# Kernel tuning notes

Hardware: AMD Instinct MI355X
Metric: run time of the kernel (lower is better)

## Reference

```python
import jax, jax.numpy as jnp
import numpy as np
import itertools

N_LEVELS = 16
F = 2
OFFSETS = [0, 4096, 12096, 27721, 60489, 124489, 249489, 511633, 1023633,
           1547921, 2072209, 2596497, 3120785, 3645073, 4169361, 4693649, 5217937]
RESOLUTIONS = [16, 20, 25, 32, 40, 50, 64, 80, 101, 128, 161, 203, 256, 322, 406, 512]
# Instant-NGP spatial hash primes (first prime = 1)
PRIMES = np.array([1, 2654435761, 805459861], dtype=np.uint32)
CORNERS = np.array(list(itertools.product([0, 1], repeat=3)), dtype=np.int32)  # (8,3)
B = 1 << 20


def setup_inputs() -> dict:
    key = jax.random.key(0)
    k1, k2 = jax.random.split(key)
    xyz = jax.random.uniform(k1, (B, 3), dtype=jnp.float32)  # points in [0,1)
    embeddings = jax.random.normal(k2, (OFFSETS[-1], F), dtype=jnp.float32) * 0.01
    return {
        'xyz': xyz,
        'embeddings': embeddings,
        'min_xyz': jnp.zeros((3,), jnp.float32),
        'max_xyz': jnp.ones((3,), jnp.float32),
    }


def _hashgrid_encode(xyz, embeddings, min_xyz, max_xyz):
    # normalize to [0,1] inside the grid bbox
    xyz_n = (xyz - min_xyz) / (max_xyz - min_xyz)  # (B,3)
    corners_u = jnp.asarray(CORNERS).astype(jnp.uint32)          # (8,3)
    corners_f = jnp.asarray(CORNERS).astype(jnp.float32)         # (8,3)
    primes = jnp.asarray(PRIMES)                                  # (3,) uint32
    outs = []
    for l in range(N_LEVELS):
        res = RESOLUTIONS[l]
        size = OFFSETS[l + 1] - OFFSETS[l]
        pos = xyz_n * (res - 1)                                   # (B,3) in [0,res-1]
        pos0 = jnp.clip(jnp.floor(pos), 0.0, res - 2)             # lower corner
        w = pos - pos0                                            # (B,3) trilinear frac
        p0 = pos0.astype(jnp.uint32)
        idx3 = p0[:, None, :] + corners_u[None]                   # (B,8,3)
        if res ** 3 <= size:
            # dense level: linear index
            idx = idx3[..., 0] * jnp.uint32(res * res) + idx3[..., 1] * jnp.uint32(res) + idx3[..., 2]
        else:
            # hashed level: xor of prime-multiplied coords (uint32 wraparound)
            idx = (idx3[..., 0] * primes[0]) ^ (idx3[..., 1] * primes[1]) ^ (idx3[..., 2] * primes[2])
            idx = idx % jnp.uint32(size)
        idx = idx.astype(jnp.int32) + OFFSETS[l]                  # (B,8) global entry id
        # trilinear weights: prod_d [ c_d ? w_d : 1-w_d ]
        wc = jnp.prod(corners_f[None] * w[:, None, :] + (1.0 - corners_f[None]) * (1.0 - w[:, None, :]), axis=-1)  # (B,8)
        feats = embeddings[idx]                                   # (B,8,F) gather
        outs.append(jnp.einsum('bc,bcf->bf', wc, feats))          # (B,F)
    return jnp.concatenate(outs, axis=-1)                         # (B, L*F)


def reference(xyz, embeddings, min_xyz, max_xyz):
    return _hashgrid_encode(xyz, embeddings, min_xyz, max_xyz)
```

## Files before the change

kernel.cpp:

```cpp
#include <hip/hip_runtime.h>
#include <stdint.h>


__device__ __constant__ int kRES[16] = {16,20,25,32,40,50,64,80,101,128,161,203,256,322,406,512};

__global__ __launch_bounds__(256, 8) void hashgrid_phased(
    const float* __restrict__ xyz,
    const float2* __restrict__ emb,
    const float* __restrict__ mn,
    const float* __restrict__ mx,
    float* __restrict__ out,
    int npts)
{
    constexpr uint32_t P1 = 2654435761u, P2 = 805459861u;
    constexpr uint32_t HASH_MASK = 0x7FFFFu;
    constexpr uint32_t HASH_BASE = 1023633u;

    const int b = blockIdx.x * blockDim.x + threadIdx.x;
    if (b >= npts) return;

    const float mn0 = mn[0], mn1 = mn[1], mn2 = mn[2];
    const float inv0 = 1.0f / (mx[0] - mn0);
    const float inv1 = 1.0f / (mx[1] - mn1);
    const float inv2 = 1.0f / (mx[2] - mn2);

    const float xn = (xyz[3*b+0] - mn0) * inv0;
    const float yn = (xyz[3*b+1] - mn1) * inv1;
    const float zn = (xyz[3*b+2] - mn2) * inv2;

    const int y = blockIdx.y;

    if (y == 0) {
        constexpr int RES[8] = {16,20,25,32,40,50,64,80};
        constexpr uint32_t OFFS[8] = {0u,4096u,12096u,27721u,60489u,124489u,249489u,511633u};
        float o[16];
#pragma unroll
        for (int l = 0; l < 8; ++l) {
            const int res = RES[l];
            const uint32_t off = OFFS[l];
            const float scale = (float)(res - 1);
            const float hi = (float)(res - 2);

            const float px = xn * scale, py = yn * scale, pz = zn * scale;
            const float fx = fminf(fmaxf(floorf(px), 0.0f), hi);
            const float fy = fminf(fmaxf(floorf(py), 0.0f), hi);
            const float fz = fminf(fmaxf(floorf(pz), 0.0f), hi);
            const float wx1 = px - fx, wy1 = py - fy, wz1 = pz - fz;
            const float wx0 = 1.0f - wx1, wy0 = 1.0f - wy1, wz0 = 1.0f - wz1;
            const uint32_t ix = (uint32_t)fx, iy = (uint32_t)fy, iz = (uint32_t)fz;

            const uint32_t dx = (uint32_t)(res * res);
            const uint32_t dy = (uint32_t)res;
            const uint32_t base = off + ix * dx + iy * dy + iz;

            float ax = 0.0f, ay = 0.0f;
            {
                float2 e0 = emb[base];           float2 e1 = emb[base + 1];
                float wxy = wx0 * wy0;
                ax += wxy * (wz0 * e0.x + wz1 * e1.x);
                ay += wxy * (wz0 * e0.y + wz1 * e1.y);
            }
            {
                float2 e0 = emb[base + dy];      float2 e1 = emb[base + dy + 1];
                float wxy = wx0 * wy1;
                ax += wxy * (wz0 * e0.x + wz1 * e1.x);
                ay += wxy * (wz0 * e0.y + wz1 * e1.y);
            }
            {
                float2 e0 = emb[base + dx];      float2 e1 = emb[base + dx + 1];
                float wxy = wx1 * wy0;
                ax += wxy * (wz0 * e0.x + wz1 * e1.x);
                ay += wxy * (wz0 * e0.y + wz1 * e1.y);
            }
            {
                float2 e0 = emb[base + dx + dy]; float2 e1 = emb[base + dx + dy + 1];
                float wxy = wx1 * wy1;
                ax += wxy * (wz0 * e0.x + wz1 * e1.x);
                ay += wxy * (wz0 * e0.y + wz1 * e1.y);
            }
            o[2*l]   = ax;
            o[2*l+1] = ay;
        }
        float4* ov = (float4*)(out + (size_t)b * 32);
#pragma unroll
        for (int i = 0; i < 4; ++i)
            ov[i] = make_float4(o[4*i+0], o[4*i+1], o[4*i+2], o[4*i+3]);
    } else {
        const int l = y + 7;
        const int res = kRES[l];
        const uint32_t off = HASH_BASE + (uint32_t)(l - 8) * 524288u;

        const float scale = (float)(res - 1);
        const float hi = (float)(res - 2);

        const float px = xn * scale, py = yn * scale, pz = zn * scale;
        const float fx = fminf(fmaxf(floorf(px), 0.0f), hi);
        const float fy = fminf(fmaxf(floorf(py), 0.0f), hi);
        const float fz = fminf(fmaxf(floorf(pz), 0.0f), hi);
        const float wx1 = px - fx, wy1 = py - fy, wz1 = pz - fz;
        const float wx0 = 1.0f - wx1, wy0 = 1.0f - wy1, wz0 = 1.0f - wz1;
        const uint32_t ix = (uint32_t)fx, iy = (uint32_t)fy, iz = (uint32_t)fz;

        const uint32_t hx0 = ix,      hx1 = ix + 1u;
        const uint32_t hy0 = iy * P1, hy1 = hy0 + P1;
        const uint32_t hz0 = iz * P2, hz1 = hz0 + P2;

        const uint32_t i000 = ((hx0 ^ hy0 ^ hz0) & HASH_MASK) + off;
        const uint32_t i001 = ((hx0 ^ hy0 ^ hz1) & HASH_MASK) + off;
        const uint32_t i010 = ((hx0 ^ hy1 ^ hz0) & HASH_MASK) + off;
        const uint32_t i011 = ((hx0 ^ hy1 ^ hz1) & HASH_MASK) + off;
        const uint32_t i100 = ((hx1 ^ hy0 ^ hz0) & HASH_MASK) + off;
        const uint32_t i101 = ((hx1 ^ hy0 ^ hz1) & HASH_MASK) + off;
        const uint32_t i110 = ((hx1 ^ hy1 ^ hz0) & HASH_MASK) + off;
        const uint32_t i111 = ((hx1 ^ hy1 ^ hz1) & HASH_MASK) + off;

        float2 e000 = emb[i000], e001 = emb[i001], e010 = emb[i010], e011 = emb[i011];
        float2 e100 = emb[i100], e101 = emb[i101], e110 = emb[i110], e111 = emb[i111];

        float ax, ay, w;
        w = wx0*wy0*wz0; ax  = w*e000.x; ay  = w*e000.y;
        w = wx0*wy0*wz1; ax += w*e001.x; ay += w*e001.y;
        w = wx0*wy1*wz0; ax += w*e010.x; ay += w*e010.y;
        w = wx0*wy1*wz1; ax += w*e011.x; ay += w*e011.y;
        w = wx1*wy0*wz0; ax += w*e100.x; ay += w*e100.y;
        w = wx1*wy0*wz1; ax += w*e101.x; ay += w*e101.y;
        w = wx1*wy1*wz0; ax += w*e110.x; ay += w*e110.y;
        w = wx1*wy1*wz1; ax += w*e111.x; ay += w*e111.y;

        float2* op = (float2*)(out + (size_t)b * 32 + 2 * l);
        *op = make_float2(ax, ay);
    }
}

extern "C" void kernel_launch(void* const* d_in, const int* in_sizes, int n_in,
                              void* d_out, int out_size, void* d_ws, size_t ws_size,
                              hipStream_t stream) {
    const float*  xyz = (const float*)d_in[0];
    const float2* emb = (const float2*)d_in[1];
    const float*  mn  = (const float*)d_in[2];
    const float*  mx  = (const float*)d_in[3];
    float* out = (float*)d_out;

    const int npts = in_sizes[0] / 3;
    const int block = 256;
    const int grid_x = (npts + block - 1) / block;

    hipLaunchKernelGGL(hashgrid_phased, dim3(grid_x, 9), dim3(block), 0, stream,
                       xyz, emb, mn, mx, out, npts);
}
```

Measured before the change: 776.9 us.

## Repack dense-level embeddings into per-cell contiguous blocks before gathering

```diff
diff --git a/kernel.cpp b/kernel.cpp
--- a/kernel.cpp
+++ b/kernel.cpp
@@ -2,9 +2,166 @@
 #include <stdint.h>
 
 
+typedef float vf4 __attribute__((ext_vector_type(4)));
+typedef float vf2 __attribute__((ext_vector_type(2)));
+
 __device__ __constant__ int kRES[16] = {16,20,25,32,40,50,64,80,101,128,161,203,256,322,406,512};
 
-__global__ __launch_bounds__(256, 8) void hashgrid_phased(
+#define D_RES   {16,20,25,32,40,50,64,80}
+#define D_OFF   {0u,4096u,12096u,27721u,60489u,124489u,249489u,511633u}
+#define D_CBASE {0u,3375u,10234u,24058u,53849u,113168u,230817u,480864u}
+#define D_CTOT  973903u
+#define D_QTOT  3895612u
+
+__device__ __constant__ uint32_t kCB[9] = {0u,3375u,10234u,24058u,53849u,113168u,230817u,480864u,973903u};
+__device__ __constant__ int      kDR[8] = D_RES;
+__device__ __constant__ uint32_t kDO[8] = D_OFF;
+
+__global__ __launch_bounds__(256) void prep_cells(
+    const float2* __restrict__ emb, float2* __restrict__ ws)
+{
+    const uint32_t tid = blockIdx.x * 256u + threadIdx.x;
+    if (tid >= D_QTOT) return;
+
+    const uint32_t cell = tid >> 2;
+    const uint32_t part = tid & 3u;
+
+    int l = 0;
+#pragma unroll
+    for (int i = 1; i < 8; ++i) l += (cell >= kCB[i]);
+
+    const uint32_t c  = cell - kCB[l];
+    const int res = kDR[l];
+    const uint32_t r1 = (uint32_t)(res - 1);
+
+    const uint32_t cz  = c % r1;
+    const uint32_t t   = c / r1;
+    const uint32_t cy  = t % r1;
+    const uint32_t cx  = t / r1;
+
+    const uint32_t bx = part >> 1, by = part & 1u;
+    const uint32_t src = kDO[l] + (cx + bx) * (uint32_t)(res * res)
+                                + (cy + by) * (uint32_t)res + cz;
+
+    const float2 e0 = emb[src];
+    const float2 e1 = emb[src + 1];
+
+    vf4 v = {e0.x, e0.y, e1.x, e1.y};
+    __builtin_nontemporal_store(v, (vf4*)(ws + ((size_t)cell * 8u + part * 2u)));
+}
+
+__global__ __launch_bounds__(256, 8) void hashgrid_cell(
+    const float* __restrict__ xyz,
+    const float2* __restrict__ emb,
+    const float2* __restrict__ ws,
+    const float* __restrict__ mn,
+    const float* __restrict__ mx,
+    float* __restrict__ out,
+    int npts)
+{
+    constexpr uint32_t P1 = 2654435761u, P2 = 805459861u;
+    constexpr uint32_t HASH_MASK = 0x7FFFFu;
+    constexpr uint32_t HASH_BASE = 1023633u;
+
+    const int b = blockIdx.x * blockDim.x + threadIdx.x;
+    if (b >= npts) return;
+
+    const float mn0 = mn[0], mn1 = mn[1], mn2 = mn[2];
+    const float inv0 = 1.0f / (mx[0] - mn0);
+    const float inv1 = 1.0f / (mx[1] - mn1);
+    const float inv2 = 1.0f / (mx[2] - mn2);
+
+    const float xn = (__builtin_nontemporal_load(&xyz[3 * b + 0]) - mn0) * inv0;
+    const float yn = (__builtin_nontemporal_load(&xyz[3 * b + 1]) - mn1) * inv1;
+    const float zn = (__builtin_nontemporal_load(&xyz[3 * b + 2]) - mn2) * inv2;
+
+    const int y = blockIdx.y;
+
+    if (y == 0) {
+        constexpr int RES[8] = D_RES;
+        constexpr uint32_t CB[8] = D_CBASE;
+        float o[16];
+#pragma unroll
+        for (int l = 0; l < 8; ++l) {
+            const int res = RES[l];
+            const uint32_t r1 = (uint32_t)(res - 1);
+            const float scale = (float)(res - 1);
+            const float hi    = (float)(res - 2);
+
+            const float px = xn * scale, py = yn * scale, pz = zn * scale;
+            const float fx = fminf(fmaxf(floorf(px), 0.0f), hi);
+            const float fy = fminf(fmaxf(floorf(py), 0.0f), hi);
+            const float fz = fminf(fmaxf(floorf(pz), 0.0f), hi);
+            const float wx1 = px - fx, wy1 = py - fy, wz1 = pz - fz;
+            const float wx0 = 1.0f - wx1, wy0 = 1.0f - wy1, wz0 = 1.0f - wz1;
+            const uint32_t ix = (uint32_t)fx, iy = (uint32_t)fy, iz = (uint32_t)fz;
+
+            const uint32_t cell = CB[l] + (ix * r1 + iy) * r1 + iz;
+            const vf4* blk = (const vf4*)(ws + (size_t)cell * 8u);
+            const vf4 q0 = blk[0], q1 = blk[1], q2 = blk[2], q3 = blk[3];
+
+            float ax, ay, w;
+            w = wx0 * wy0; ax  = w * (wz0 * q0.x + wz1 * q0.z); ay  = w * (wz0 * q0.y + wz1 * q0.w);
+            w = wx0 * wy1; ax += w * (wz0 * q1.x + wz1 * q1.z); ay += w * (wz0 * q1.y + wz1 * q1.w);
+            w = wx1 * wy0; ax += w * (wz0 * q2.x + wz1 * q2.z); ay += w * (wz0 * q2.y + wz1 * q2.w);
+            w = wx1 * wy1; ax += w * (wz0 * q3.x + wz1 * q3.z); ay += w * (wz0 * q3.y + wz1 * q3.w);
+            o[2 * l]     = ax;
+            o[2 * l + 1] = ay;
+        }
+        float* op = out + (size_t)b * 32;
+#pragma unroll
+        for (int i = 0; i < 4; ++i) {
+            vf4 v = {o[4 * i + 0], o[4 * i + 1], o[4 * i + 2], o[4 * i + 3]};
+            __builtin_nontemporal_store(v, (vf4*)(op + 4 * i));
+        }
+    } else {
+        const int l = y + 7;
+        const int res = kRES[l];
+        const uint32_t off = HASH_BASE + (uint32_t)(l - 8) * 524288u;
+
+        const float scale = (float)(res - 1);
+        const float hi    = (float)(res - 2);
+
+        const float px = xn * scale, py = yn * scale, pz = zn * scale;
+        const float fx = fminf(fmaxf(floorf(px), 0.0f), hi);
+        const float fy = fminf(fmaxf(floorf(py), 0.0f), hi);
+        const float fz = fminf(fmaxf(floorf(pz), 0.0f), hi);
+        const float wx1 = px - fx, wy1 = py - fy, wz1 = pz - fz;
+        const float wx0 = 1.0f - wx1, wy0 = 1.0f - wy1, wz0 = 1.0f - wz1;
+        const uint32_t ix = (uint32_t)fx, iy = (uint32_t)fy, iz = (uint32_t)fz;
+
+        const uint32_t hx0 = ix,      hx1 = ix + 1u;
+        const uint32_t hy0 = iy * P1, hy1 = hy0 + P1;
+        const uint32_t hz0 = iz * P2, hz1 = hz0 + P2;
+
+        const uint32_t i000 = ((hx0 ^ hy0 ^ hz0) & HASH_MASK) + off;
+        const uint32_t i001 = ((hx0 ^ hy0 ^ hz1) & HASH_MASK) + off;
+        const uint32_t i010 = ((hx0 ^ hy1 ^ hz0) & HASH_MASK) + off;
+        const uint32_t i011 = ((hx0 ^ hy1 ^ hz1) & HASH_MASK) + off;
+        const uint32_t i100 = ((hx1 ^ hy0 ^ hz0) & HASH_MASK) + off;
+        const uint32_t i101 = ((hx1 ^ hy0 ^ hz1) & HASH_MASK) + off;
+        const uint32_t i110 = ((hx1 ^ hy1 ^ hz0) & HASH_MASK) + off;
+        const uint32_t i111 = ((hx1 ^ hy1 ^ hz1) & HASH_MASK) + off;
+
+        const float2 e000 = emb[i000], e001 = emb[i001], e010 = emb[i010], e011 = emb[i011];
+        const float2 e100 = emb[i100], e101 = emb[i101], e110 = emb[i110], e111 = emb[i111];
+
+        float ax, ay, w;
+        w = wx0 * wy0 * wz0; ax  = w * e000.x; ay  = w * e000.y;
+        w = wx0 * wy0 * wz1; ax += w * e001.x; ay += w * e001.y;
+        w = wx0 * wy1 * wz0; ax += w * e010.x; ay += w * e010.y;
+        w = wx0 * wy1 * wz1; ax += w * e011.x; ay += w * e011.y;
+        w = wx1 * wy0 * wz0; ax += w * e100.x; ay += w * e100.y;
+        w = wx1 * wy0 * wz1; ax += w * e101.x; ay += w * e101.y;
+        w = wx1 * wy1 * wz0; ax += w * e110.x; ay += w * e110.y;
+        w = wx1 * wy1 * wz1; ax += w * e111.x; ay += w * e111.y;
+
+        vf2 v = {ax, ay};
+        __builtin_nontemporal_store(v, (vf2*)(out + (size_t)b * 32 + 2 * l));
+    }
+}
+
+__global__ __launch_bounds__(256, 8) void hashgrid_direct(
     const float* __restrict__ xyz,
     const float2* __restrict__ emb,
     const float* __restrict__ mn,
@@ -24,15 +181,15 @@
     const float inv1 = 1.0f / (mx[1] - mn1);
     const float inv2 = 1.0f / (mx[2] - mn2);
 
-    const float xn = (xyz[3*b+0] - mn0) * inv0;
-    const float yn = (xyz[3*b+1] - mn1) * inv1;
-    const float zn = (xyz[3*b+2] - mn2) * inv2;
+    const float xn = (xyz[3 * b + 0] - mn0) * inv0;
+    const float yn = (xyz[3 * b + 1] - mn1) * inv1;
+    const float zn = (xyz[3 * b + 2] - mn2) * inv2;
 
     const int y = blockIdx.y;
 
     if (y == 0) {
-        constexpr int RES[8] = {16,20,25,32,40,50,64,80};
-        constexpr uint32_t OFFS[8] = {0u,4096u,12096u,27721u,60489u,124489u,249489u,511633u};
+        constexpr int RES[8] = D_RES;
+        constexpr uint32_t OFFS[8] = D_OFF;
         float o[16];
 #pragma unroll
         for (int l = 0; l < 8; ++l) {
@@ -57,34 +214,30 @@
             {
                 float2 e0 = emb[base];           float2 e1 = emb[base + 1];
                 float wxy = wx0 * wy0;
-                ax += wxy * (wz0 * e0.x + wz1 * e1.x);
-                ay += wxy * (wz0 * e0.y + wz1 * e1.y);
+                ax += wxy * (wz0 * e0.x + wz1 * e1.x); ay += wxy * (wz0 * e0.y + wz1 * e1.y);
             }
             {
                 float2 e0 = emb[base + dy];      float2 e1 = emb[base + dy + 1];
                 float wxy = wx0 * wy1;
-                ax += wxy * (wz0 * e0.x + wz1 * e1.x);
-                ay += wxy * (wz0 * e0.y + wz1 * e1.y);
+                ax += wxy * (wz0 * e0.x + wz1 * e1.x); ay += wxy * (wz0 * e0.y + wz1 * e1.y);
             }
             {
                 float2 e0 = emb[base + dx];      float2 e1 = emb[base + dx + 1];
                 float wxy = wx1 * wy0;
-                ax += wxy * (wz0 * e0.x + wz1 * e1.x);
-                ay += wxy * (wz0 * e0.y + wz1 * e1.y);
+                ax += wxy * (wz0 * e0.x + wz1 * e1.x); ay += wxy * (wz0 * e0.y + wz1 * e1.y);
             }
             {
                 float2 e0 = emb[base + dx + dy]; float2 e1 = emb[base + dx + dy + 1];
                 float wxy = wx1 * wy1;
-                ax += wxy * (wz0 * e0.x + wz1 * e1.x);
-                ay += wxy * (wz0 * e0.y + wz1 * e1.y);
+                ax += wxy * (wz0 * e0.x + wz1 * e1.x); ay += wxy * (wz0 * e0.y + wz1 * e1.y);
             }
-            o[2*l]   = ax;
-            o[2*l+1] = ay;
+            o[2 * l]     = ax;
+            o[2 * l + 1] = ay;
         }
         float4* ov = (float4*)(out + (size_t)b * 32);
 #pragma unroll
         for (int i = 0; i < 4; ++i)
-            ov[i] = make_float4(o[4*i+0], o[4*i+1], o[4*i+2], o[4*i+3]);
+            ov[i] = make_float4(o[4 * i + 0], o[4 * i + 1], o[4 * i + 2], o[4 * i + 3]);
     } else {
         const int l = y + 7;
         const int res = kRES[l];
@@ -114,18 +267,18 @@
         const uint32_t i110 = ((hx1 ^ hy1 ^ hz0) & HASH_MASK) + off;
         const uint32_t i111 = ((hx1 ^ hy1 ^ hz1) & HASH_MASK) + off;
 
-        float2 e000 = emb[i000], e001 = emb[i001], e010 = emb[i010], e011 = emb[i011];
-        float2 e100 = emb[i100], e101 = emb[i101], e110 = emb[i110], e111 = emb[i111];
+        const float2 e000 = emb[i000], e001 = emb[i001], e010 = emb[i010], e011 = emb[i011];
+        const float2 e100 = emb[i100], e101 = emb[i101], e110 = emb[i110], e111 = emb[i111];
 
         float ax, ay, w;
-        w = wx0*wy0*wz0; ax  = w*e000.x; ay  = w*e000.y;
-        w = wx0*wy0*wz1; ax += w*e001.x; ay += w*e001.y;
-        w = wx0*wy1*wz0; ax += w*e010.x; ay += w*e010.y;
-        w = wx0*wy1*wz1; ax += w*e011.x; ay += w*e011.y;
-        w = wx1*wy0*wz0; ax += w*e100.x; ay += w*e100.y;
-        w = wx1*wy0*wz1; ax += w*e101.x; ay += w*e101.y;
-        w = wx1*wy1*wz0; ax += w*e110.x; ay += w*e110.y;
-        w = wx1*wy1*wz1; ax += w*e111.x; ay += w*e111.y;
+        w = wx0 * wy0 * wz0; ax  = w * e000.x; ay  = w * e000.y;
+        w = wx0 * wy0 * wz1; ax += w * e001.x; ay += w * e001.y;
+        w = wx0 * wy1 * wz0; ax += w * e010.x; ay += w * e010.y;
+        w = wx0 * wy1 * wz1; ax += w * e011.x; ay += w * e011.y;
+        w = wx1 * wy0 * wz0; ax += w * e100.x; ay += w * e100.y;
+        w = wx1 * wy0 * wz1; ax += w * e101.x; ay += w * e101.y;
+        w = wx1 * wy1 * wz0; ax += w * e110.x; ay += w * e110.y;
+        w = wx1 * wy1 * wz1; ax += w * e111.x; ay += w * e111.y;
 
         float2* op = (float2*)(out + (size_t)b * 32 + 2 * l);
         *op = make_float2(ax, ay);
@@ -145,6 +298,16 @@
     const int block = 256;
     const int grid_x = (npts + block - 1) / block;
 
-    hipLaunchKernelGGL(hashgrid_phased, dim3(grid_x, 9), dim3(block), 0, stream,
-                       xyz, emb, mn, mx, out, npts);
+    const size_t ws_needed = (size_t)D_CTOT * 64u;
+
+    if (ws_size >= ws_needed && d_ws != nullptr) {
+        float2* ws = (float2*)d_ws;
+        const int prep_grid = (int)((D_QTOT + 255u) / 256u);
+        hipLaunchKernelGGL(prep_cells, dim3(prep_grid), dim3(256), 0, stream, emb, ws);
+        hipLaunchKernelGGL(hashgrid_cell, dim3(grid_x, 9), dim3(block), 0, stream,
+                           xyz, emb, ws, mn, mx, out, npts);
+    } else {
+        hipLaunchKernelGGL(hashgrid_direct, dim3(grid_x, 9), dim3(block), 0, stream,
+                           xyz, emb, mn, mx, out, npts);
+    }
 }
```

After: 748.2 us. 1.04x faster.
